# Performance work log

Measured on AMD Instinct MI355X. Metric: run time of the kernel, lower is better.

The kernel has to match this reference:

```python
import jax, jax.numpy as jnp
import numpy as np

N_LAYERS = 2
D_MODEL = 1024
D_INNER = 2 * D_MODEL
D_STATE = 16
D_CONV = 4
DT_RANK = D_MODEL // 16  # 64
B_SZ, L = 1, 2048
EPS = 1e-5


def layernorm(x, w, b):
    mu = jnp.mean(x, axis=-1, keepdims=True)
    var = jnp.mean(jnp.square(x - mu), axis=-1, keepdims=True)
    return (x - mu) * jax.lax.rsqrt(var + EPS) * w + b


def mamba(x, in_w, cw, cb, xp_w, dtp_w, dtp_b, A_log, Dp, out_w):
    # x: [B, L, D_MODEL]
    Bn, Ln, _ = x.shape
    xz = jnp.einsum('bld,ed->ble', x, in_w)          # [B,L,2*D_INNER]
    xc, z = jnp.split(xz, 2, axis=-1)
    # causal depthwise conv1d (kernel D_CONV)
    xp = jnp.pad(xc, ((0, 0), (D_CONV - 1, 0), (0, 0)))
    xc = sum(xp[:, k:k + Ln, :] * cw[:, k] for k in range(D_CONV)) + cb
    xc = jax.nn.silu(xc)
    dbl = jnp.einsum('ble,re->blr', xc, xp_w)        # [B,L,DT_RANK+2*D_STATE]
    dt, Bm, Cm = jnp.split(dbl, [DT_RANK, DT_RANK + D_STATE], axis=-1)
    dt = jax.nn.softplus(jnp.einsum('blr,er->ble', dt, dtp_w) + dtp_b)  # [B,L,E]
    A = -jnp.exp(A_log)                              # [E,N], strictly negative
    dA = jnp.exp(dt[..., None] * A)                  # [B,L,E,N]
    dBu = (dt * xc)[..., None] * Bm[:, :, None, :]   # [B,L,E,N]

    def step(h, inp):
        dA_t, dBu_t, C_t = inp
        h = dA_t * h + dBu_t                         # [B,E,N]
        y = jnp.einsum('ben,bn->be', h, C_t)
        return h, y

    h0 = jnp.zeros((Bn, D_INNER, D_STATE), dA.dtype)
    _, ys = jax.lax.scan(step, h0, (dA.transpose(1, 0, 2, 3),
                                    dBu.transpose(1, 0, 2, 3),
                                    Cm.transpose(1, 0, 2)))
    y = ys.transpose(1, 0, 2) + xc * Dp              # [B,L,E]
    y = y * jax.nn.silu(z)
    return jnp.einsum('ble,de->bld', y, out_w)       # [B,L,D_MODEL]


def setup_inputs() -> dict:
    key = jax.random.key(0)
    ks = jax.random.split(key, 12)
    s = 0.02
    dt_init = np.log(np.expm1(0.01)).astype(np.float32)  # softplus^-1(0.01)
    A_row = jnp.log(jnp.arange(1, D_STATE + 1, dtype=jnp.float32))
    return {
        'x': jax.random.normal(ks[0], (B_SZ, L, D_MODEL), jnp.float32),
        'ln_w': jnp.ones((N_LAYERS, D_MODEL), jnp.float32),
        'ln_b': jnp.zeros((N_LAYERS, D_MODEL), jnp.float32),
        'in_proj_w': jax.random.normal(ks[1], (N_LAYERS, 2 * D_INNER, D_MODEL)) * s,
        'conv_w': jax.random.normal(ks[2], (N_LAYERS, D_INNER, D_CONV)) * 0.2,
        'conv_b': jnp.zeros((N_LAYERS, D_INNER), jnp.float32),
        'x_proj_w': jax.random.normal(ks[3], (N_LAYERS, DT_RANK + 2 * D_STATE, D_INNER)) * s,
        'dt_proj_w': jax.random.normal(ks[4], (N_LAYERS, D_INNER, DT_RANK)) * (DT_RANK ** -0.5),
        'dt_proj_b': jnp.full((N_LAYERS, D_INNER), dt_init),
        'A_log': jnp.broadcast_to(A_row, (N_LAYERS, D_INNER, D_STATE)).copy(),
        'D_skip': jnp.ones((N_LAYERS, D_INNER), jnp.float32),
        'out_proj_w': jax.random.normal(ks[5], (N_LAYERS, D_MODEL, D_INNER)) * s,
        'norm_f_w': jnp.ones((D_MODEL,), jnp.float32),
        'norm_f_b': jnp.zeros((D_MODEL,), jnp.float32),
    }


def reference(x, ln_w, ln_b, in_proj_w, conv_w, conv_b, x_proj_w, dt_proj_w,
              dt_proj_b, A_log, D_skip, out_proj_w, norm_f_w, norm_f_b):
    for i in range(N_LAYERS):
        h = layernorm(x, ln_w[i], ln_b[i])
        h = mamba(h, in_proj_w[i], conv_w[i], conv_b[i], x_proj_w[i],
                  dt_proj_w[i], dt_proj_b[i], A_log[i], D_skip[i], out_proj_w[i])
        x = h + x  # residual (dropout/drop_path are identity in eval)
    return layernorm(x, norm_f_w, norm_f_b)
```

## Files before the change

kernel.cpp:

```cpp
#include <hip/hip_runtime.h>
#include <hip/hip_cooperative_groups.h>
#include <hip/hip_bf16.h>
#include <math.h>

namespace cg = cooperative_groups;

#define LSEQ 2048
#define DMODEL 1024
#define DINNER 2048
#define DSTATE 16
#define DCONV 4
#define DTRANK 64
#define RPROJ 96

#define CHUNK 16
#define NCHUNK (LSEQ / CHUNK)

#define XSPLIT 4
#define NBLK 512

typedef __attribute__((ext_vector_type(8))) short bf16x8;
typedef __attribute__((ext_vector_type(4))) float f32x4;

__device__ __forceinline__ float softplusf(float x) {
    return (x > 20.f) ? x : log1pf(__expf(x));
}
__device__ __forceinline__ float siluf(float x) {
    return x / (1.f + __expf(-x));
}
__device__ __forceinline__ short f2bf(float f) {
    union { float f; unsigned u; } v; v.f = f;
    unsigned r = v.u + 0x7FFFu + ((v.u >> 16) & 1u);
    return (short)(r >> 16);
}
__device__ __forceinline__ float bf2f(short h) {
    union { unsigned u; float f; } v;
    v.u = ((unsigned)(unsigned short)h) << 16;
    return v.f;
}

__device__ __forceinline__ void cvt8(const float* __restrict__ s,
                                     short* __restrict__ d, int i) {
    const float4 a = *(const float4*)(s + i);
    const float4 b = *(const float4*)(s + i + 4);
    alignas(16) short h[8];
    h[0] = f2bf(a.x); h[1] = f2bf(a.y); h[2] = f2bf(a.z); h[3] = f2bf(a.w);
    h[4] = f2bf(b.x); h[5] = f2bf(b.y); h[6] = f2bf(b.z); h[7] = f2bf(b.w);
    *(uint4*)(d + i) = *(const uint4*)h;
}

__device__ __forceinline__ void cvt_phase(
    const float* __restrict__ in_w, short* __restrict__ in_w_bf,
    const float* __restrict__ xp_w, short* __restrict__ xp_w_bf,
    const float* __restrict__ out_w, short* __restrict__ out_w_bf,
    const float* __restrict__ dtp_w, short* __restrict__ dtp_w_bf,
    int g0, int gstride)
{
    const int n1 = 2 * (2 * DINNER) * DMODEL;
    const int n2 = 2 * RPROJ * DINNER;
    const int n3 = 2 * DMODEL * DINNER;
    const int n4 = 2 * DINNER * DTRANK;
    const int total8 = (n1 + n2 + n3 + n4) / 8;
    for (int g = g0; g < total8; g += gstride) {
        int i = g * 8;
        if (i < n1) { cvt8(in_w, in_w_bf, i); continue; }
        i -= n1;
        if (i < n2) { cvt8(xp_w, xp_w_bf, i); continue; }
        i -= n2;
        if (i < n3) { cvt8(out_w, out_w_bf, i); continue; }
        i -= n3;
        cvt8(dtp_w, dtp_w_bf, i);
    }
}

__device__ __forceinline__ void ln_phase(
    const float* __restrict__ x, const float* __restrict__ w,
    const float* __restrict__ b, float* __restrict__ outf,
    short* __restrict__ outb, int bid, int tid)
{
    const int wv = tid >> 6, lane = tid & 63;
    const int row = bid * 4 + wv;
    const float* xr = x + (size_t)row * DMODEL;
    float v[16];
    float s = 0.f, sq = 0.f;
#pragma unroll
    for (int k = 0; k < 16; k++) {
        v[k] = xr[k * 64 + lane];
        s += v[k];
        sq += v[k] * v[k];
    }
#pragma unroll
    for (int off = 32; off > 0; off >>= 1) {
        s += __shfl_xor(s, off, 64);
        sq += __shfl_xor(sq, off, 64);
    }
    const float mu = s * (1.f / DMODEL);
    const float var = sq * (1.f / DMODEL) - mu * mu;
    const float rstd = rsqrtf(var + 1e-5f);
#pragma unroll
    for (int k = 0; k < 16; k++) {
        const int i = k * 64 + lane;
        const float o = (v[k] - mu) * rstd * w[i] + b[i];
        if (outf) outf[(size_t)row * DMODEL + i] = o;
        else      outb[(size_t)row * DMODEL + i] = f2bf(o);
    }
}

template<int MI, int NJ, int MODE>
__device__ __forceinline__ void gemm_phase(
    unsigned char* smemraw,
    const short* __restrict__ A, int lda,
    const short* __restrict__ W, int ldw,
    float* __restrict__ Cf, short* __restrict__ Cb, int ldc,
    int N, int K, int row0, int col0, int kbeg,
    const float* __restrict__ resid, int tid)
{
    constexpr int BM = 32 * MI;
    constexpr int BN = 32 * NJ;
    constexpr int AISS = BM / 32;
    constexpr int WISS = BN / 32;
    short* As = (short*)smemraw;
    short* Ws = (short*)(smemraw + (size_t)BM * 64 * 2);

    const int lane = tid & 63;
    const int w = tid >> 6;
    const int wr = w >> 1, wc = w & 1;
    const int srow = tid >> 3;
    const int dch  = tid & 7;
    const int skch = (dch ^ (srow & 7)) * 8;

    f32x4 acc[MI][NJ];
#pragma unroll
    for (int i = 0; i < MI; i++)
#pragma unroll
        for (int j = 0; j < NJ; j++) acc[i][j] = (f32x4)0.f;

    const int lrow = lane & 15;
    const int q = lane >> 4;

    for (int kt = kbeg; kt < kbeg + K; kt += 64) {
        __syncthreads();
#pragma unroll
        for (int j = 0; j < AISS; j++) {
            const short* gp = A + (size_t)(row0 + j * 32 + srow) * lda + kt + skch;
            __builtin_amdgcn_global_load_lds(
                (const __attribute__((address_space(1))) void*)gp,
                (__attribute__((address_space(3))) void*)(&As[j * 2048 + tid * 8]),
                16, 0, 0);
        }
#pragma unroll
        for (int j = 0; j < WISS; j++) {
            const int wrow = col0 + j * 32 + srow;
            if (wrow < N) {
                const short* gp = W + (size_t)wrow * ldw + kt + skch;
                __builtin_amdgcn_global_load_lds(
                    (const __attribute__((address_space(1))) void*)gp,
                    (__attribute__((address_space(3))) void*)(&Ws[j * 2048 + tid * 8]),
                    16, 0, 0);
            }
        }
        __syncthreads();

#pragma unroll
        for (int ks = 0; ks < 2; ks++) {
            bf16x8 af[MI], bfr[NJ];
#pragma unroll
            for (int i = 0; i < MI; i++) {
                const int R = wr * (16 * MI) + i * 16 + lrow;
                const int pc = (ks * 4 + q) ^ (R & 7);
                af[i] = *(const bf16x8*)&As[R * 64 + pc * 8];
            }
#pragma unroll
            for (int j = 0; j < NJ; j++) {
                const int R = wc * (16 * NJ) + j * 16 + lrow;
                const int pc = (ks * 4 + q) ^ (R & 7);
                bfr[j] = *(const bf16x8*)&Ws[R * 64 + pc * 8];
            }
#pragma unroll
            for (int i = 0; i < MI; i++)
#pragma unroll
                for (int j = 0; j < NJ; j++)
                    acc[i][j] = __builtin_amdgcn_mfma_f32_16x16x32_bf16(
                        af[i], bfr[j], acc[i][j], 0, 0, 0);
        }
    }

    const int rbase = row0 + wr * (16 * MI);
    const int cbase = col0 + wc * (16 * NJ);
#pragma unroll
    for (int i = 0; i < MI; i++) {
#pragma unroll
        for (int j = 0; j < NJ; j++) {
            const int gcol = cbase + j * 16 + lrow;
            if (gcol < N) {
#pragma unroll
                for (int r = 0; r < 4; r++) {
                    const int grow = rbase + i * 16 + (lane >> 4) * 4 + r;
                    float v = acc[i][j][r];
                    if (MODE == 2) {
                        Cf[(size_t)grow * ldc + gcol] =
                            v + resid[(size_t)grow * ldc + gcol];
                    } else if (MODE == 3) {
                        Cb[(size_t)grow * ldc + gcol] = f2bf(v);
                    } else {
                        atomicAdd(&Cf[(size_t)grow * ldc + gcol], v);
                    }
                }
            }
        }
    }
}

__device__ __forceinline__ void dtproj_phase(
    unsigned char* smemraw,
    const float* __restrict__ dbl,
    const short* __restrict__ dtp_w,
    const float* __restrict__ dtp_b,
    short* __restrict__ dt_bf,
    int row0, int col0, int tid)
{
    short* As = (short*)smemraw;
    short* Ws = (short*)(smemraw + 64 * 32 * 2);
    const int lane = tid & 63;
    const int w = tid >> 6;
    const int wr = w >> 1, wc = w & 1;
    const int srow = tid >> 2;
    const int skch = ((tid & 3) ^ ((srow >> 1) & 3)) * 8;
    const int lrow = lane & 15;
    const int q = lane >> 4;

    f32x4 acc[2][4];
#pragma unroll
    for (int i = 0; i < 2; i++)
#pragma unroll
        for (int j = 0; j < 4; j++) acc[i][j] = (f32x4)0.f;

#pragma unroll
    for (int kt = 0; kt < 64; kt += 32) {
        __syncthreads();
        {
            const float* gp = dbl + (size_t)(row0 + srow) * RPROJ + kt + skch;
            const float4 a = *(const float4*)gp;
            const float4 b = *(const float4*)(gp + 4);
            alignas(16) short h[8];
            h[0] = f2bf(a.x); h[1] = f2bf(a.y); h[2] = f2bf(a.z); h[3] = f2bf(a.w);
            h[4] = f2bf(b.x); h[5] = f2bf(b.y); h[6] = f2bf(b.z); h[7] = f2bf(b.w);
            *(uint4*)(As + tid * 8) = *(const uint4*)h;
        }
#pragma unroll
        for (int j = 0; j < 2; j++) {
            const short* gp = dtp_w + (size_t)(col0 + j * 64 + srow) * DTRANK + kt + skch;
            __builtin_amdgcn_global_load_lds(
                (const __attribute__((address_space(1))) void*)gp,
                (__attribute__((address_space(3))) void*)(&Ws[j * 2048 + tid * 8]),
                16, 0, 0);
        }
        __syncthreads();

        bf16x8 af[2], bfr[4];
#pragma unroll
        for (int i = 0; i < 2; i++) {
            const int R = wr * 32 + i * 16 + lrow;
            af[i] = *(const bf16x8*)&As[R * 32 + ((q ^ ((R >> 1) & 3)) * 8)];
        }
#pragma unroll
        for (int j = 0; j < 4; j++) {
            const int R = wc * 64 + j * 16 + lrow;
            bfr[j] = *(const bf16x8*)&Ws[R * 32 + ((q ^ ((R >> 1) & 3)) * 8)];
        }
#pragma unroll
        for (int i = 0; i < 2; i++)
#pragma unroll
            for (int j = 0; j < 4; j++)
                acc[i][j] = __builtin_amdgcn_mfma_f32_16x16x32_bf16(
                    af[i], bfr[j], acc[i][j], 0, 0, 0);
    }

    const int rbase = row0 + wr * 32;
    const int cbase = col0 + wc * 64;
#pragma unroll
    for (int i = 0; i < 2; i++)
#pragma unroll
        for (int j = 0; j < 4; j++) {
            const int gcol = cbase + j * 16 + lrow;
#pragma unroll
            for (int r = 0; r < 4; r++) {
                const int grow = rbase + i * 16 + (lane >> 4) * 4 + r;
                dt_bf[(size_t)grow * DINNER + gcol] =
                    f2bf(softplusf(acc[i][j][r] + dtp_b[gcol]));
            }
        }
}

__device__ __forceinline__ void conv_phase(
    const short* __restrict__ xzb, const float* __restrict__ cw,
    const float* __restrict__ cb, short* __restrict__ xcb,
    float* __restrict__ dbl_zero, int gid0, int gstride)
{
    for (int g = gid0; g < (LSEQ * DINNER) / 8; g += gstride) {
        if (g < (LSEQ * RPROJ) / 4)
            *(float4*)(dbl_zero + g * 4) = make_float4(0.f, 0.f, 0.f, 0.f);
        const int t = g >> 8;
        const int c0 = (g & 255) * 8;
        float acc[8];
#pragma unroll
        for (int j = 0; j < 8; j++) acc[j] = cb[c0 + j];
#pragma unroll
        for (int k = 0; k < DCONV; k++) {
            const int tt = t - (DCONV - 1) + k;
            if (tt >= 0) {
                const bf16x8 v = *(const bf16x8*)(xzb + (size_t)tt * (2 * DINNER) + c0);
#pragma unroll
                for (int j = 0; j < 8; j++)
                    acc[j] += bf2f(v[j]) * cw[(c0 + j) * DCONV + k];
            }
        }
        alignas(16) short h[8];
#pragma unroll
        for (int j = 0; j < 8; j++) h[j] = f2bf(siluf(acc[j]));
        *(uint4*)(xcb + (size_t)t * DINNER + c0) = *(const uint4*)h;
    }
}

__device__ __forceinline__ void scan1_job(
    int eb, int c, int tid, float* sBC,
    const short* __restrict__ dtb, const short* __restrict__ xcb,
    const float* __restrict__ dbl, const float* __restrict__ A_log,
    float* __restrict__ S, float* __restrict__ sumdt)
{
    const int e = eb * 256 + tid;
    float a[DSTATE];
#pragma unroll
    for (int n = 0; n < DSTATE; n++) a[n] = -__expf(A_log[(size_t)e * DSTATE + n]);
    float h[DSTATE];
#pragma unroll
    for (int n = 0; n < DSTATE; n++) h[n] = 0.f;
    float sd = 0.f;

    __syncthreads();
    for (int i = tid; i < CHUNK * 32; i += 256) {
        const int tl = i >> 5, j = i & 31;
        sBC[tl * 32 + j] = dbl[(size_t)(c * CHUNK + tl) * RPROJ + DTRANK + j];
    }
    __syncthreads();

    const size_t rb = (size_t)c * CHUNK * DINNER + e;
    short dt_c = dtb[rb], xc_c = xcb[rb];
#pragma unroll
    for (int tl = 0; tl < CHUNK; tl++) {
        short dt_n = 0, xc_n = 0;
        if (tl + 1 < CHUNK) {
            dt_n = dtb[rb + (size_t)(tl + 1) * DINNER];
            xc_n = xcb[rb + (size_t)(tl + 1) * DINNER];
        }
        const float dtv = bf2f(dt_c);
        const float du = dtv * bf2f(xc_c);
        sd += dtv;
#pragma unroll
        for (int n = 0; n < DSTATE; n++) {
            const float dA = __expf(dtv * a[n]);
            h[n] = dA * h[n] + du * sBC[tl * 32 + n];
        }
        dt_c = dt_n; xc_c = xc_n;
    }
    sumdt[(size_t)c * DINNER + e] = sd;
#pragma unroll
    for (int n = 0; n < DSTATE; n++)
        S[((size_t)c * DSTATE + n) * DINNER + e] = h[n];
}

__device__ __forceinline__ void scan2_phase(
    const float* __restrict__ A_log, const float* __restrict__ sumdt,
    float* __restrict__ S, int idx)
{
    const int e = idx & (DINNER - 1);
    const int n = idx >> 11;
    const float a = -__expf(A_log[(size_t)e * DSTATE + n]);
    const size_t base = (size_t)n * DINNER + e;
    const size_t cstr = (size_t)DSTATE * DINNER;
    float H = 0.f;
    for (int c = 0; c < NCHUNK; c += 4) {
        const float sc0 = S[base + (size_t)(c + 0) * cstr];
        const float sc1 = S[base + (size_t)(c + 1) * cstr];
        const float sc2 = S[base + (size_t)(c + 2) * cstr];
        const float sc3 = S[base + (size_t)(c + 3) * cstr];
        const float sd0 = sumdt[(size_t)(c + 0) * DINNER + e];
        const float sd1 = sumdt[(size_t)(c + 1) * DINNER + e];
        const float sd2 = sumdt[(size_t)(c + 2) * DINNER + e];
        const float sd3 = sumdt[(size_t)(c + 3) * DINNER + e];
        S[base + (size_t)(c + 0) * cstr] = H;
        H = __expf(a * sd0) * H + sc0;
        S[base + (size_t)(c + 1) * cstr] = H;
        H = __expf(a * sd1) * H + sc1;
        S[base + (size_t)(c + 2) * cstr] = H;
        H = __expf(a * sd2) * H + sc2;
        S[base + (size_t)(c + 3) * cstr] = H;
        H = __expf(a * sd3) * H + sc3;
    }
}

__device__ __forceinline__ void scan3_job(
    int eb, int c, int tid, float* sBC,
    const short* __restrict__ dtb, const short* __restrict__ xcb,
    const float* __restrict__ dbl, const short* __restrict__ xzb,
    const float* __restrict__ A_log, const float* __restrict__ Dp,
    const float* __restrict__ S, short* __restrict__ yb)
{
    const int e = eb * 256 + tid;
    float a[DSTATE];
#pragma unroll
    for (int n = 0; n < DSTATE; n++) a[n] = -__expf(A_log[(size_t)e * DSTATE + n]);
    float h[DSTATE];
#pragma unroll
    for (int n = 0; n < DSTATE; n++)
        h[n] = S[((size_t)c * DSTATE + n) * DINNER + e];
    const float dskip = Dp[e];

    __syncthreads();
    for (int i = tid; i < CHUNK * 32; i += 256) {
        const int tl = i >> 5, j = i & 31;
        sBC[tl * 32 + j] = dbl[(size_t)(c * CHUNK + tl) * RPROJ + DTRANK + j];
    }
    __syncthreads();

    const size_t rb = (size_t)c * CHUNK * DINNER + e;
    const size_t zb = (size_t)c * CHUNK * (2 * DINNER) + DINNER + e;
    short dt_c = dtb[rb], xc_c = xcb[rb], z_c = xzb[zb];
#pragma unroll
    for (int tl = 0; tl < CHUNK; tl++) {
        short dt_n = 0, xc_n = 0, z_n = 0;
        if (tl + 1 < CHUNK) {
            dt_n = dtb[rb + (size_t)(tl + 1) * DINNER];
            xc_n = xcb[rb + (size_t)(tl + 1) * DINNER];
            z_n = xzb[zb + (size_t)(tl + 1) * (2 * DINNER)];
        }
        const float dtv = bf2f(dt_c);
        const float xcv = bf2f(xc_c);
        const float du = dtv * xcv;
        float yv = 0.f;
#pragma unroll
        for (int n = 0; n < DSTATE; n++) {
            const float dA = __expf(dtv * a[n]);
            h[n] = dA * h[n] + du * sBC[tl * 32 + n];
            yv += h[n] * sBC[tl * 32 + 16 + n];
        }
        yv = (yv + xcv * dskip) * siluf(bf2f(z_c));
        yb[rb + (size_t)tl * DINNER] = f2bf(yv);
        dt_c = dt_n; xc_c = xc_n; z_c = z_n;
    }
}

struct MegaParams {
    const float *x_in, *ln_w, *ln_b, *in_w, *conv_w, *conv_b, *xp_w, *dtp_w,
                *dtp_b, *A_log, *D_skip, *out_w, *nf_w, *nf_b;
    float* out;
    float *buf_x, *dbl, *Sbuf, *sumdt;
    short *h_bf, *xz_bf, *xc_bf, *dt_bf, *y_bf;
    short *in_w_bf, *xp_w_bf, *dtp_w_bf, *out_w_bf;
};

__global__ __launch_bounds__(256, 2) void mega_kernel(MegaParams p)
{
    cg::grid_group grid = cg::this_grid();
    __shared__ alignas(16) unsigned char smem[32768];
    const int bid = blockIdx.x;
    const int tid = threadIdx.x;

    cvt_phase(p.in_w, p.in_w_bf, p.xp_w, p.xp_w_bf, p.out_w, p.out_w_bf,
              p.dtp_w, p.dtp_w_bf, bid * 256 + tid, NBLK * 256);
    grid.sync();

    for (int layer = 0; layer < 2; layer++) {
        const float* resid = layer ? p.buf_x : p.x_in;
        ln_phase(resid, p.ln_w + layer * DMODEL, p.ln_b + layer * DMODEL,
                 nullptr, p.h_bf, bid, tid);
        grid.sync();
        {
            const int swz = (bid & 7) * 64 + (bid >> 3);
            const int tx = swz & 31, ty = swz >> 5;
            gemm_phase<4, 4, 3>(smem,
                p.h_bf, DMODEL,
                p.in_w_bf + (size_t)layer * 2 * DINNER * DMODEL, DMODEL,
                nullptr, p.xz_bf, 2 * DINNER,
                2 * DINNER, DMODEL, ty * 128, tx * 128, 0, nullptr, tid);
        }
        grid.sync();
        conv_phase(p.xz_bf, p.conv_w + (size_t)layer * DINNER * DCONV,
                   p.conv_b + layer * DINNER, p.xc_bf, p.dbl,
                   bid * 256 + tid, NBLK * 256);
        grid.sync();
        if (bid < 2 * 32 * XSPLIT) {
            const int jx = bid & 1, jy = (bid >> 1) & 31, jz = bid >> 6;
            gemm_phase<2, 2, 6>(smem,
                p.xc_bf, DINNER,
                p.xp_w_bf + (size_t)layer * RPROJ * DINNER, DINNER,
                p.dbl, nullptr, RPROJ,
                RPROJ, DINNER / XSPLIT, jy * 64, jx * 64,
                jz * (DINNER / XSPLIT), nullptr, tid);
        }
        grid.sync();
        {
            const int jx = bid & 15, jy = bid >> 4;
            dtproj_phase(smem, p.dbl,
                         p.dtp_w_bf + (size_t)layer * DINNER * DTRANK,
                         p.dtp_b + layer * DINNER, p.dt_bf,
                         jy * 64, jx * 128, tid);
        }
        grid.sync();
        {
            const float* Al = p.A_log + (size_t)layer * DINNER * DSTATE;
            float* sBC = (float*)smem;
#pragma unroll
            for (int jj = 0; jj < 2; jj++) {
                const int job = bid * 2 + jj;
                scan1_job(job & 7, job >> 3, tid, sBC,
                          p.dt_bf, p.xc_bf, p.dbl, Al, p.Sbuf, p.sumdt);
            }
        }
        grid.sync();
        if (bid < (DINNER * DSTATE) / 256) {
            const float* Al = p.A_log + (size_t)layer * DINNER * DSTATE;
            scan2_phase(Al, p.sumdt, p.Sbuf, bid * 256 + tid);
        }
        grid.sync();
        {
            const float* Al = p.A_log + (size_t)layer * DINNER * DSTATE;
            float* sBC = (float*)smem;
#pragma unroll
            for (int jj = 0; jj < 2; jj++) {
                const int job = bid * 2 + jj;
                scan3_job(job & 7, job >> 3, tid, sBC,
                          p.dt_bf, p.xc_bf, p.dbl, p.xz_bf, Al,
                          p.D_skip + layer * DINNER, p.Sbuf, p.y_bf);
            }
        }
        grid.sync();
        {
            const int swz = (bid & 7) * 64 + (bid >> 3);
            const int jx = swz & 15, jy = swz >> 4;
            gemm_phase<2, 2, 2>(smem,
                p.y_bf, DINNER,
                p.out_w_bf + (size_t)layer * DMODEL * DINNER, DINNER,
                p.buf_x, nullptr, DMODEL,
                DMODEL, DINNER, jy * 64, jx * 64, 0, resid, tid);
        }
        grid.sync();
    }
    ln_phase(p.buf_x, p.nf_w, p.nf_b, p.out, nullptr, bid, tid);
}

__global__ __launch_bounds__(256) void cvt_g(
    const float* in_w, short* in_w_bf, const float* xp_w, short* xp_w_bf,
    const float* out_w, short* out_w_bf, const float* dtp_w, short* dtp_w_bf)
{
    cvt_phase(in_w, in_w_bf, xp_w, xp_w_bf, out_w, out_w_bf, dtp_w, dtp_w_bf,
              blockIdx.x * 256 + threadIdx.x, gridDim.x * 256);
}

__global__ __launch_bounds__(256) void ln_g(
    const float* x, const float* w, const float* b, float* outf, short* outb)
{
    ln_phase(x, w, b, outf, outb, blockIdx.x, threadIdx.x);
}

template<int MI, int NJ, int MODE>
__global__ __launch_bounds__(256) void gemm_g(
    const short* A, int lda, const short* W, int ldw,
    float* Cf, short* Cb, int ldc, int N, int K, const float* resid)
{
    __shared__ alignas(16) unsigned char smem[(32 * MI + 32 * NJ) * 64 * 2];
    gemm_phase<MI, NJ, MODE>(smem, A, lda, W, ldw, Cf, Cb, ldc, N, K,
                             blockIdx.y * 32 * MI, blockIdx.x * 32 * NJ,
                             blockIdx.z * K, resid, threadIdx.x);
}

__global__ __launch_bounds__(256) void conv_g(
    const short* xzb, const float* cw, const float* cb, short* xcb,
    float* dbl_zero)
{
    conv_phase(xzb, cw, cb, xcb, dbl_zero,
               blockIdx.x * 256 + threadIdx.x, gridDim.x * 256);
}

__global__ __launch_bounds__(256) void dtproj_g(
    const float* dbl, const short* dtp_w, const float* dtp_b, short* dt_bf)
{
    __shared__ alignas(16) unsigned char smem[(64 + 128) * 32 * 2];
    dtproj_phase(smem, dbl, dtp_w, dtp_b, dt_bf,
                 blockIdx.y * 64, blockIdx.x * 128, threadIdx.x);
}

__global__ __launch_bounds__(256) void scan1_g(
    const short* dtb, const short* xcb, const float* dbl,
    const float* A_log, float* S, float* sumdt)
{
    __shared__ float sBC[CHUNK * 32];
    scan1_job(blockIdx.x, blockIdx.y, threadIdx.x, sBC,
              dtb, xcb, dbl, A_log, S, sumdt);
}

__global__ __launch_bounds__(256) void scan2_g(
    const float* A_log, const float* sumdt, float* S)
{
    scan2_phase(A_log, sumdt, S, blockIdx.x * 256 + threadIdx.x);
}

__global__ __launch_bounds__(256) void scan3_g(
    const short* dtb, const short* xcb, const float* dbl, const short* xzb,
    const float* A_log, const float* Dp, const float* S, short* yb)
{
    __shared__ float sBC[CHUNK * 32];
    scan3_job(blockIdx.x, blockIdx.y, threadIdx.x, sBC,
              dtb, xcb, dbl, xzb, A_log, Dp, S, yb);
}

extern "C" void kernel_launch(void* const* d_in, const int* in_sizes, int n_in,
                              void* d_out, int out_size, void* d_ws, size_t ws_size,
                              hipStream_t stream) {
    float* w = (float*)d_ws;
    float* buf_x = w; w += (size_t)LSEQ * DMODEL;
    float* dbl   = w; w += (size_t)LSEQ * RPROJ;
    float* Sbuf  = w; w += (size_t)NCHUNK * DSTATE * DINNER;
    float* sumdt = w; w += (size_t)NCHUNK * DINNER;
    short* h_bf    = (short*)w; w += (size_t)LSEQ * DMODEL / 2;
    short* xz_bf   = (short*)w; w += (size_t)LSEQ * 2 * DINNER / 2;
    short* xc_bf   = (short*)w; w += (size_t)LSEQ * DINNER / 2;
    short* dt_bf   = (short*)w; w += (size_t)LSEQ * DINNER / 2;
    short* y_bf    = (short*)w; w += (size_t)LSEQ * DINNER / 2;
    short* in_w_bf  = (short*)w; w += (size_t)2 * (2 * DINNER) * DMODEL / 2;
    short* xp_w_bf  = (short*)w; w += (size_t)2 * RPROJ * DINNER / 2;
    short* dtp_w_bf = (short*)w; w += (size_t)2 * DINNER * DTRANK / 2;
    short* out_w_bf = (short*)w; w += (size_t)2 * DMODEL * DINNER / 2;

    MegaParams p;
    p.x_in   = (const float*)d_in[0];
    p.ln_w   = (const float*)d_in[1];
    p.ln_b   = (const float*)d_in[2];
    p.in_w   = (const float*)d_in[3];
    p.conv_w = (const float*)d_in[4];
    p.conv_b = (const float*)d_in[5];
    p.xp_w   = (const float*)d_in[6];
    p.dtp_w  = (const float*)d_in[7];
    p.dtp_b  = (const float*)d_in[8];
    p.A_log  = (const float*)d_in[9];
    p.D_skip = (const float*)d_in[10];
    p.out_w  = (const float*)d_in[11];
    p.nf_w   = (const float*)d_in[12];
    p.nf_b   = (const float*)d_in[13];
    p.out    = (float*)d_out;
    p.buf_x = buf_x; p.dbl = dbl; p.Sbuf = Sbuf; p.sumdt = sumdt;
    p.h_bf = h_bf; p.xz_bf = xz_bf; p.xc_bf = xc_bf; p.dt_bf = dt_bf;
    p.y_bf = y_bf;
    p.in_w_bf = in_w_bf; p.xp_w_bf = xp_w_bf; p.dtp_w_bf = dtp_w_bf;
    p.out_w_bf = out_w_bf;

    static int coop_state = -1;
    if (coop_state == -1) {
        int dev = 0;
        (void)hipGetDevice(&dev);
        hipDeviceProp_t prop;
        int nb = 0;
        if (hipGetDeviceProperties(&prop, dev) == hipSuccess &&
            hipOccupancyMaxActiveBlocksPerMultiprocessor(
                &nb, (const void*)mega_kernel, 256, 0) == hipSuccess &&
            nb * prop.multiProcessorCount >= NBLK) {
            coop_state = 1;
        } else {
            coop_state = 0;
        }
    }
    if (coop_state == 1) {
        void* args[] = { &p };
        hipError_t e = hipLaunchCooperativeKernel(
            (void*)mega_kernel, dim3(NBLK), dim3(256), args, 0, stream);
        if (e == hipSuccess) return;
        (void)hipGetLastError();
        coop_state = 0;
    }

    cvt_g<<<dim3(6464), dim3(256), 0, stream>>>(
        p.in_w, in_w_bf, p.xp_w, xp_w_bf, p.out_w, out_w_bf, p.dtp_w, dtp_w_bf);
    for (int layer = 0; layer < 2; layer++) {
        const float* resid_src = (layer == 0) ? p.x_in : buf_x;
        ln_g<<<dim3(NBLK), dim3(256), 0, stream>>>(
            resid_src, p.ln_w + layer * DMODEL, p.ln_b + layer * DMODEL,
            nullptr, h_bf);
        gemm_g<4, 4, 3><<<dim3(32, 16), dim3(256), 0, stream>>>(
            h_bf, DMODEL, in_w_bf + (size_t)layer * 2 * DINNER * DMODEL, DMODEL,
            nullptr, xz_bf, 2 * DINNER, 2 * DINNER, DMODEL, nullptr);
        conv_g<<<dim3(2048), dim3(256), 0, stream>>>(
            xz_bf, p.conv_w + (size_t)layer * DINNER * DCONV,
            p.conv_b + layer * DINNER, xc_bf, dbl);
        gemm_g<2, 2, 6><<<dim3(2, 32, XSPLIT), dim3(256), 0, stream>>>(
            xc_bf, DINNER, xp_w_bf + (size_t)layer * RPROJ * DINNER, DINNER,
            dbl, nullptr, RPROJ, RPROJ, DINNER / XSPLIT, nullptr);
        dtproj_g<<<dim3(16, 32), dim3(256), 0, stream>>>(
            dbl, dtp_w_bf + (size_t)layer * DINNER * DTRANK,
            p.dtp_b + layer * DINNER, dt_bf);
        const float* Al = p.A_log + (size_t)layer * DINNER * DSTATE;
        scan1_g<<<dim3(8, NCHUNK), dim3(256), 0, stream>>>(
            dt_bf, xc_bf, dbl, Al, Sbuf, sumdt);
        scan2_g<<<dim3((DINNER * DSTATE) / 256), dim3(256), 0, stream>>>(
            Al, sumdt, Sbuf);
        scan3_g<<<dim3(8, NCHUNK), dim3(256), 0, stream>>>(
            dt_bf, xc_bf, dbl, xz_bf, Al, p.D_skip + layer * DINNER, Sbuf, y_bf);
        gemm_g<2, 2, 2><<<dim3(16, 32), dim3(256), 0, stream>>>(
            y_bf, DINNER, out_w_bf + (size_t)layer * DMODEL * DINNER, DINNER,
            buf_x, nullptr, DMODEL, DMODEL, DINNER, resid_src);
    }
    ln_g<<<dim3(NBLK), dim3(256), 0, stream>>>(buf_x, p.nf_w, p.nf_b,
                                               (float*)d_out, nullptr);
}
```

Baseline: 481.7 us.

## Split cooperative megakernel into per-layer group kernels and double scan chunk

```diff
diff --git a/kernel.cpp b/kernel.cpp
--- a/kernel.cpp
+++ b/kernel.cpp
@@ -13,7 +13,7 @@
 #define DTRANK 64
 #define RPROJ 96
 
-#define CHUNK 16
+#define CHUNK 32
 #define NCHUNK (LSEQ / CHUNK)
 
 #define XSPLIT 4
@@ -346,7 +346,7 @@
 
     const size_t rb = (size_t)c * CHUNK * DINNER + e;
     short dt_c = dtb[rb], xc_c = xcb[rb];
-#pragma unroll
+#pragma unroll 4
     for (int tl = 0; tl < CHUNK; tl++) {
         short dt_n = 0, xc_n = 0;
         if (tl + 1 < CHUNK) {
@@ -426,7 +426,7 @@
     const size_t rb = (size_t)c * CHUNK * DINNER + e;
     const size_t zb = (size_t)c * CHUNK * (2 * DINNER) + DINNER + e;
     short dt_c = dtb[rb], xc_c = xcb[rb], z_c = xzb[zb];
-#pragma unroll
+#pragma unroll 4
     for (int tl = 0; tl < CHUNK; tl++) {
         short dt_n = 0, xc_n = 0, z_n = 0;
         if (tl + 1 < CHUNK) {
@@ -459,94 +459,67 @@
     short *in_w_bf, *xp_w_bf, *dtp_w_bf, *out_w_bf;
 };
 
-__global__ __launch_bounds__(256, 2) void mega_kernel(MegaParams p)
+__global__ __launch_bounds__(256, 2) void groupA_kernel(MegaParams p, int layer)
 {
     cg::grid_group grid = cg::this_grid();
     __shared__ alignas(16) unsigned char smem[32768];
     const int bid = blockIdx.x;
     const int tid = threadIdx.x;
-
-    cvt_phase(p.in_w, p.in_w_bf, p.xp_w, p.xp_w_bf, p.out_w, p.out_w_bf,
-              p.dtp_w, p.dtp_w_bf, bid * 256 + tid, NBLK * 256);
+    const float* resid = layer ? p.buf_x : p.x_in;
+
+    ln_phase(resid, p.ln_w + layer * DMODEL, p.ln_b + layer * DMODEL,
+             nullptr, p.h_bf, bid, tid);
     grid.sync();
-
-    for (int layer = 0; layer < 2; layer++) {
-        const float* resid = layer ? p.buf_x : p.x_in;
-        ln_phase(resid, p.ln_w + layer * DMODEL, p.ln_b + layer * DMODEL,
-                 nullptr, p.h_bf, bid, tid);
-        grid.sync();
-        {
-            const int swz = (bid & 7) * 64 + (bid >> 3);
-            const int tx = swz & 31, ty = swz >> 5;
-            gemm_phase<4, 4, 3>(smem,
-                p.h_bf, DMODEL,
-                p.in_w_bf + (size_t)layer * 2 * DINNER * DMODEL, DMODEL,
-                nullptr, p.xz_bf, 2 * DINNER,
-                2 * DINNER, DMODEL, ty * 128, tx * 128, 0, nullptr, tid);
-        }
-        grid.sync();
-        conv_phase(p.xz_bf, p.conv_w + (size_t)layer * DINNER * DCONV,
-                   p.conv_b + layer * DINNER, p.xc_bf, p.dbl,
-                   bid * 256 + tid, NBLK * 256);
-        grid.sync();
-        if (bid < 2 * 32 * XSPLIT) {
-            const int jx = bid & 1, jy = (bid >> 1) & 31, jz = bid >> 6;
-            gemm_phase<2, 2, 6>(smem,
-                p.xc_bf, DINNER,
-                p.xp_w_bf + (size_t)layer * RPROJ * DINNER, DINNER,
-                p.dbl, nullptr, RPROJ,
-                RPROJ, DINNER / XSPLIT, jy * 64, jx * 64,
-                jz * (DINNER / XSPLIT), nullptr, tid);
-        }
-        grid.sync();
-        {
-            const int jx = bid & 15, jy = bid >> 4;
-            dtproj_phase(smem, p.dbl,
-                         p.dtp_w_bf + (size_t)layer * DINNER * DTRANK,
-                         p.dtp_b + layer * DINNER, p.dt_bf,
-                         jy * 64, jx * 128, tid);
-        }
-        grid.sync();
-        {
-            const float* Al = p.A_log + (size_t)layer * DINNER * DSTATE;
-            float* sBC = (float*)smem;
-#pragma unroll
-            for (int jj = 0; jj < 2; jj++) {
-                const int job = bid * 2 + jj;
-                scan1_job(job & 7, job >> 3, tid, sBC,
-                          p.dt_bf, p.xc_bf, p.dbl, Al, p.Sbuf, p.sumdt);
-            }
-        }
-        grid.sync();
-        if (bid < (DINNER * DSTATE) / 256) {
-            const float* Al = p.A_log + (size_t)layer * DINNER * DSTATE;
-            scan2_phase(Al, p.sumdt, p.Sbuf, bid * 256 + tid);
-        }
-        grid.sync();
-        {
-            const float* Al = p.A_log + (size_t)layer * DINNER * DSTATE;
-            float* sBC = (float*)smem;
-#pragma unroll
-            for (int jj = 0; jj < 2; jj++) {
-                const int job = bid * 2 + jj;
-                scan3_job(job & 7, job >> 3, tid, sBC,
-                          p.dt_bf, p.xc_bf, p.dbl, p.xz_bf, Al,
-                          p.D_skip + layer * DINNER, p.Sbuf, p.y_bf);
-            }
-        }
-        grid.sync();
-        {
-            const int swz = (bid & 7) * 64 + (bid >> 3);
-            const int jx = swz & 15, jy = swz >> 4;
-            gemm_phase<2, 2, 2>(smem,
-                p.y_bf, DINNER,
-                p.out_w_bf + (size_t)layer * DMODEL * DINNER, DINNER,
-                p.buf_x, nullptr, DMODEL,
-                DMODEL, DINNER, jy * 64, jx * 64, 0, resid, tid);
-        }
-        grid.sync();
-    }
-    ln_phase(p.buf_x, p.nf_w, p.nf_b, p.out, nullptr, bid, tid);
+    {
+        const int swz = (bid & 7) * 64 + (bid >> 3);
+        const int tx = swz & 31, ty = swz >> 5;
+        gemm_phase<4, 4, 3>(smem,
+            p.h_bf, DMODEL,
+            p.in_w_bf + (size_t)layer * 2 * DINNER * DMODEL, DMODEL,
+            nullptr, p.xz_bf, 2 * DINNER,
+            2 * DINNER, DMODEL, ty * 128, tx * 128, 0, nullptr, tid);
+    }
+    grid.sync();
+    conv_phase(p.xz_bf, p.conv_w + (size_t)layer * DINNER * DCONV,
+               p.conv_b + layer * DINNER, p.xc_bf, p.dbl,
+               bid * 256 + tid, NBLK * 256);
+}
+
+__global__ __launch_bounds__(256, 2) void groupB_kernel(MegaParams p, int layer)
+{
+    cg::grid_group grid = cg::this_grid();
+    __shared__ alignas(16) unsigned char smem[16384];
+    const int bid = blockIdx.x;
+    const int tid = threadIdx.x;
+    const float* Al = p.A_log + (size_t)layer * DINNER * DSTATE;
+
+    if (bid < 2 * 32 * XSPLIT) {
+        const int jx = bid & 1, jy = (bid >> 1) & 31, jz = bid >> 6;
+        gemm_phase<2, 2, 6>(smem,
+            p.xc_bf, DINNER,
+            p.xp_w_bf + (size_t)layer * RPROJ * DINNER, DINNER,
+            p.dbl, nullptr, RPROJ,
+            RPROJ, DINNER / XSPLIT, jy * 64, jx * 64,
+            jz * (DINNER / XSPLIT), nullptr, tid);
+    }
+    grid.sync();
+    {
+        const int jx = bid & 15, jy = bid >> 4;
+        dtproj_phase(smem, p.dbl,
+                     p.dtp_w_bf + (size_t)layer * DINNER * DTRANK,
+                     p.dtp_b + layer * DINNER, p.dt_bf,
+                     jy * 64, jx * 128, tid);
+    }
+    grid.sync();
+    scan1_job(bid & 7, bid >> 3, tid, (float*)smem,
+              p.dt_bf, p.xc_bf, p.dbl, Al, p.Sbuf, p.sumdt);
+    grid.sync();
+    if (bid < (DINNER * DSTATE) / 256)
+        scan2_phase(Al, p.sumdt, p.Sbuf, bid * 256 + tid);
+    grid.sync();
+    scan3_job(bid & 7, bid >> 3, tid, (float*)smem,
+              p.dt_bf, p.xc_bf, p.dbl, p.xz_bf, Al,
+              p.D_skip + layer * DINNER, p.Sbuf, p.y_bf);
 }
 
 __global__ __launch_bounds__(256) void cvt_g(
@@ -659,21 +632,44 @@
         int dev = 0;
         (void)hipGetDevice(&dev);
         hipDeviceProp_t prop;
-        int nb = 0;
+        int na = 0, nb = 0;
         if (hipGetDeviceProperties(&prop, dev) == hipSuccess &&
             hipOccupancyMaxActiveBlocksPerMultiprocessor(
-                &nb, (const void*)mega_kernel, 256, 0) == hipSuccess &&
+                &na, (const void*)groupA_kernel, 256, 0) == hipSuccess &&
+            hipOccupancyMaxActiveBlocksPerMultiprocessor(
+                &nb, (const void*)groupB_kernel, 256, 0) == hipSuccess &&
+            na * prop.multiProcessorCount >= NBLK &&
             nb * prop.multiProcessorCount >= NBLK) {
             coop_state = 1;
         } else {
             coop_state = 0;
         }
     }
-    if (coop_state == 1) {
-        void* args[] = { &p };
-        hipError_t e = hipLaunchCooperativeKernel(
-            (void*)mega_kernel, dim3(NBLK), dim3(256), args, 0, stream);
-        if (e == hipSuccess) return;
+
+    bool ok = (coop_state == 1);
+    if (ok) {
+        cvt_g<<<dim3(6464), dim3(256), 0, stream>>>(
+            p.in_w, in_w_bf, p.xp_w, xp_w_bf, p.out_w, out_w_bf,
+            p.dtp_w, dtp_w_bf);
+        for (int layer = 0; layer < 2 && ok; layer++) {
+            int lyr = layer;
+            void* args[] = { &p, &lyr };
+            if (hipLaunchCooperativeKernel((void*)groupA_kernel, dim3(NBLK),
+                                           dim3(256), args, 0, stream)
+                != hipSuccess) { ok = false; break; }
+            if (hipLaunchCooperativeKernel((void*)groupB_kernel, dim3(NBLK),
+                                           dim3(256), args, 0, stream)
+                != hipSuccess) { ok = false; break; }
+            const float* resid_src = (layer == 0) ? p.x_in : buf_x;
+            gemm_g<2, 2, 2><<<dim3(16, 32), dim3(256), 0, stream>>>(
+                y_bf, DINNER, out_w_bf + (size_t)layer * DMODEL * DINNER,
+                DINNER, buf_x, nullptr, DMODEL, DMODEL, DINNER, resid_src);
+        }
+        if (ok) {
+            ln_g<<<dim3(NBLK), dim3(256), 0, stream>>>(
+                buf_x, p.nf_w, p.nf_b, (float*)d_out, nullptr);
+            return;
+        }
         (void)hipGetLastError();
         coop_state = 0;
     }
```

Result: slower. 1.182 ms (+145.3%).
